# Kernel optimization log

Hardware: AMD Instinct MI355X
Metric: run time of the kernel (lower is better)

## Reference

```python
import jax, jax.numpy as jnp
import numpy as np

B, N, E = 2, 8192, 131072
IN_C, NF = 4, 32
F_IN = IN_C * NF          # 128, = in_channels * num_features
HID, H, OUT = 64, 8, 64   # hidden_features, nheads, out_features
NEG_SLOPE = 0.2           # GATv2Conv default negative_slope


def setup_inputs() -> dict:
    key = jax.random.key(0)
    ks = jax.random.split(key, 12)
    x = jax.random.normal(ks[0], (B, N, IN_C, NF), dtype=jnp.float32)
    edge_index = jax.random.randint(ks[1], (2, E), 0, N, dtype=jnp.int32)

    def w(k, shape, fan_in):
        return jax.random.normal(k, shape, dtype=jnp.float32) / np.sqrt(fan_in).astype(np.float32)

    # GATv2 layer 1: lin_l (source), lin_r (target), attention vector a, bias
    W1l = w(ks[2], (F_IN, H * HID), F_IN)
    W1r = w(ks[3], (F_IN, H * HID), F_IN)
    att1 = w(ks[4], (H, HID), HID)
    b1 = jnp.zeros((H * HID,), dtype=jnp.float32)
    # GATv2 layer 2: input channels = H*HID = 512
    W2l = w(ks[5], (H * HID, H * OUT), H * HID)
    W2r = w(ks[6], (H * HID, H * OUT), H * HID)
    att2 = w(ks[7], (H, OUT), OUT)
    b2 = jnp.zeros((H * OUT,), dtype=jnp.float32)
    return {"x": x, "edge_index": edge_index,
            "W1l": W1l, "W1r": W1r, "att1": att1, "b1": b1,
            "W2l": W2l, "W2r": W2r, "att2": att2, "b2": b2}


def _gatv2_layer(f, src, dst, Wl, Wr, att, b, heads, ch):
    # f: [N, F_in]; src/dst: [E'] (self-loops included)
    xl = (f @ Wl).reshape(N, heads, ch)   # source-side transform (messages)
    xr = (f @ Wr).reshape(N, heads, ch)   # target-side transform
    e = jax.nn.leaky_relu(xl[src] + xr[dst], NEG_SLOPE)     # [E', H, C]
    logits = jnp.einsum('ehc,hc->eh', e, att)               # [E', H]
    # softmax over incoming edges of each target node
    m = jax.lax.stop_gradient(jax.ops.segment_max(logits, dst, num_segments=N))
    a = jnp.exp(logits - m[dst])
    denom = jax.ops.segment_sum(a, dst, num_segments=N)     # [N, H] (>0: self-loops)
    a = a / denom[dst]
    out = jax.ops.segment_sum(xl[src] * a[:, :, None], dst, num_segments=N)
    return out.reshape(N, heads * ch) + b


def reference(x, edge_index, W1l, W1r, att1, b1, W2l, W2r, att2, b2):
    # add self-loops (PyG GATv2Conv default add_self_loops=True)
    loops = jnp.arange(N, dtype=edge_index.dtype)
    src = jnp.concatenate([edge_index[0], loops])
    dst = jnp.concatenate([edge_index[1], loops])
    feats = x.reshape(B, N, F_IN)  # view(batch, nodes, in_channels*num_features)

    def per_graph(f):
        h = _gatv2_layer(f, src, dst, W1l, W1r, att1, b1, H, HID)   # [N, 512]
        return _gatv2_layer(h, src, dst, W2l, W2r, att2, b2, H, OUT)  # [N, 512]

    h_prime = jax.vmap(per_graph)(feats)   # [B, N, H*OUT]
    return jax.nn.elu(h_prime)             # concat=True branch
```

## Files before the change

### kernel.cpp

```cpp
#include <hip/hip_runtime.h>
#include <cstdint>

#define NN 8192
#define NT 16384
#define EE 131072
#define EPAD (EE + NN)
#define SPAD (EPAD + 3 * NN)
#define FIN 128
#define CH 512
#define NH 8
#define NEG 0.2f

typedef __attribute__((ext_vector_type(8))) short short8;
typedef __attribute__((ext_vector_type(4))) unsigned short u16x4;
typedef __attribute__((ext_vector_type(4))) float f32x4;
typedef __attribute__((ext_vector_type(4))) int i32x4;

__device__ inline unsigned short bf16rne(float x) {
    unsigned u = __float_as_uint(x);
    unsigned r = (u + 0x7FFFu + ((u >> 16) & 1u)) >> 16;
    return (unsigned short)r;
}
__device__ inline float bf16tof(unsigned short h) {
    return __uint_as_float((unsigned)h << 16);
}
__device__ inline void gload16(const void* g, void* l) {
    __builtin_amdgcn_global_load_lds((const __attribute__((address_space(1))) void*)g,
                                     (__attribute__((address_space(3))) void*)l, 16, 0, 0);
}
template <int CTRL>
__device__ inline float dpp_add(float x) {
    int v = __builtin_amdgcn_update_dpp(0, __float_as_int(x), CTRL, 0xF, 0xF, true);
    return x + __int_as_float(v);
}


__global__ __launch_bounds__(256) void k_deg(const int* __restrict__ ei, int* __restrict__ deg) {
    int e = blockIdx.x * 256 + threadIdx.x;
    if (e >= EPAD) return;
    int dst = (e < EE) ? ei[EE + e] : (e - EE);
    atomicAdd(&deg[dst], 1);
}

__global__ __launch_bounds__(1024) void k_scan(const int* __restrict__ deg, int* __restrict__ rowptr) {
    __shared__ int part[1024];
    int t = threadIdx.x;
    int loc[8];
    int s = 0;
#pragma unroll
    for (int i = 0; i < 8; i++) { loc[i] = s; s += (deg[t * 8 + i] + 3) & ~3; }
    part[t] = s;
    __syncthreads();
    if (t == 0) {
        int run = 0;
        for (int i = 0; i < 1024; i++) { int tmp = part[i]; part[i] = run; run += tmp; }
        rowptr[NN] = run;
    }
    __syncthreads();
    int base = part[t];
#pragma unroll
    for (int i = 0; i < 8; i++) rowptr[t * 8 + i] = base + loc[i];
}

__global__ __launch_bounds__(256) void k_scatter(const int* __restrict__ ei, const int* __restrict__ rowptr,
                                                 int* __restrict__ cursor, int* __restrict__ ssrc) {
    int e = blockIdx.x * 256 + threadIdx.x;
    if (e >= EPAD) return;
    int src = (e < EE) ? ei[e] : (e - EE);
    int dst = (e < EE) ? ei[EE + e] : (e - EE);
    int pos = rowptr[dst] + atomicAdd(&cursor[dst], 1);
    ssrc[pos] = src;
}

__global__ __launch_bounds__(256) void k_pad(const int* __restrict__ rowptr, const int* __restrict__ deg,
                                             int* __restrict__ ssrc) {
    int n = blockIdx.x * 256 + threadIdx.x;
    if (n >= NN) return;
    int e = rowptr[n] + deg[n], pe = rowptr[n + 1];
    for (int i = e; i < pe; i++) ssrc[i] = 0;
}


__global__ __launch_bounds__(256) void k_cvt_ah(const float* __restrict__ F,
                                                unsigned short* __restrict__ Ah, int n4) {
    int i = blockIdx.x * 256 + threadIdx.x;
    if (i >= n4) return;
    f32x4 v = ((const f32x4*)F)[i];
#pragma unroll
    for (int c = 0; c < 4; c++) Ah[i * 4 + c] = bf16rne(v[c]);
}

template <int K>
__global__ __launch_bounds__(256) void k_cvt_w(const float* __restrict__ Wl, const float* __restrict__ Wr,
                                               unsigned short* __restrict__ Wh, unsigned short* __restrict__ Wlo) {
    int idx = blockIdx.x * 256 + threadIdx.x;
    int n = idx / K, k = idx % K;
    const float* W = (n < 512) ? Wl : Wr;
    float x = W[k * 512 + (n & 511)];
    unsigned short h = bf16rne(x);
    Wh[idx] = h;
    Wlo[idx] = bf16rne(x - bf16tof(h));
}


template <int K, int USE_BL, int BK>
__global__ __launch_bounds__(256) void k_gemm_mfma(const unsigned short* __restrict__ Ah,
                                                   const unsigned short* __restrict__ Bh,
                                                   const unsigned short* __restrict__ Bl,
                                                   unsigned short* __restrict__ XLb,
                                                   float* __restrict__ XR) {
    const int NS = BK / 8;
    __shared__ unsigned short sAh[NS][128][8], sBh[NS][128][8];
    __shared__ unsigned short sBl[USE_BL ? NS : 1][128][8];
    int tid = threadIdx.x;
    int l = tid & 63;
    int w = tid >> 6, wm = w >> 1, wn = w & 1;
    int m0 = blockIdx.x * 128, n0 = blockIdx.y * 128;
    int lr = l & 15, kh = l >> 4;
    f32x4 acc[4][4] = {};

    for (int k0 = 0; k0 < K; k0 += BK) {
#pragma unroll
        for (int g = 0; g < NS / 2; g++) {
            int cell = g * 256 + tid;
            int ckh = cell >> 7, cr = cell & 127;
            int ka = k0 + ckh * 8;
            gload16(Ah + (size_t)(m0 + cr) * K + ka, &sAh[ckh][cr][0]);
            gload16(Bh + (size_t)(n0 + cr) * K + ka, &sBh[ckh][cr][0]);
            if (USE_BL) gload16(Bl + (size_t)(n0 + cr) * K + ka, &sBl[ckh][cr][0]);
        }
        __syncthreads();
#pragma unroll
        for (int kk = 0; kk < BK / 32; kk++) {
            int ks = kk * 4 + kh;
            short8 fah[4], fbh[4], fbl[4];
#pragma unroll
            for (int i = 0; i < 4; i++) {
                fah[i] = *(const short8*)&sAh[ks][wm * 64 + i * 16 + lr][0];
                fbh[i] = *(const short8*)&sBh[ks][wn * 64 + i * 16 + lr][0];
                if (USE_BL) fbl[i] = *(const short8*)&sBl[ks][wn * 64 + i * 16 + lr][0];
            }
#pragma unroll
            for (int i = 0; i < 4; i++)
#pragma unroll
                for (int j = 0; j < 4; j++) {
                    if (USE_BL)
                        acc[i][j] = __builtin_amdgcn_mfma_f32_16x16x32_bf16(fah[i], fbl[j], acc[i][j], 0, 0, 0);
                    acc[i][j] = __builtin_amdgcn_mfma_f32_16x16x32_bf16(fah[i], fbh[j], acc[i][j], 0, 0, 0);
                }
        }
        __syncthreads();
    }
    int colt = n0 + wn * 64;
    int cb = colt & 511;
    if (colt < 512) {
#pragma unroll
        for (int i = 0; i < 4; i++) {
            int mg = m0 + wm * 64 + i * 16 + kh * 4;
#pragma unroll
            for (int j = 0; j < 4; j++) {
                int cg = cb + j * 16 + lr;
#pragma unroll
                for (int q = 0; q < 4; q++)
                    XLb[(size_t)(mg + q) * CH + cg] = bf16rne(acc[i][j][q]);
            }
        }
    } else {
#pragma unroll
        for (int i = 0; i < 4; i++) {
            int mg = m0 + wm * 64 + i * 16 + kh * 4;
#pragma unroll
            for (int j = 0; j < 4; j++) {
                int cg = cb + j * 16 + lr;
#pragma unroll
                for (int q = 0; q < 4; q++)
                    XR[(size_t)(mg + q) * CH + cg] = acc[i][j][q];
            }
        }
    }
}


#define GATHER(CX, IV)                                                         \
  {                                                                            \
    CX[0] = *(const u16x4*)(XLg + (size_t)IV[0] * CH);                         \
    CX[1] = *(const u16x4*)(XLg + (size_t)IV[1] * CH);                         \
    CX[2] = *(const u16x4*)(XLg + (size_t)IV[2] * CH);                         \
    CX[3] = *(const u16x4*)(XLg + (size_t)IV[3] * CH);                         \
  }

#define PROCESS(CX, cb)                                                        \
  {                                                                            \
    float f[4][4];                                                             \
    _Pragma("unroll") for (int e = 0; e < 4; e++)                              \
      _Pragma("unroll") for (int r = 0; r < 4; r++)                            \
        f[e][r] = bf16tof(CX[e][r]);                                           \
    float z[4];                                                                \
    _Pragma("unroll") for (int e = 0; e < 4; e++) {                            \
      float s = 0.f;                                                           \
      _Pragma("unroll") for (int r = 0; r < 4; r++) {                          \
        float t = f[e][r] + xrv[r];                                            \
        t = fmaxf(t, NEG * t);                                                 \
        s += t * atv[r];                                                       \
      }                                                                        \
      z[e] = s;                                                                \
    }                                                                          \
    _Pragma("unroll") for (int e = 0; e < 4; e++) {                            \
      z[e] = dpp_add<0xB1>(z[e]);                                              \
      z[e] = dpp_add<0x4E>(z[e]);                                              \
      z[e] = dpp_add<0x124>(z[e]);                                             \
      z[e] = dpp_add<0x128>(z[e]);                                             \
    }                                                                          \
    _Pragma("unroll") for (int e = 1; e < 4; e++)                              \
      if ((cb) + e >= end) z[e] = -1e30f;                                      \
    float mc = fmaxf(fmaxf(z[0], z[1]), fmaxf(z[2], z[3]));                    \
    if (__ballot(mc > mh + 8.f) == 0ULL) {                                     \
      float p0 = __expf(z[0] - mh), p1 = __expf(z[1] - mh);                    \
      float p2 = __expf(z[2] - mh), p3 = __expf(z[3] - mh);                    \
      sh += (p0 + p1) + (p2 + p3);                                             \
      _Pragma("unroll") for (int r = 0; r < 4; r++)                            \
        acc[r] += p0 * f[0][r] + p1 * f[1][r] + p2 * f[2][r] + p3 * f[3][r];   \
    } else {                                                                   \
      float nm = fmaxf(mh, mc);                                                \
      float sc = __expf(mh - nm);                                              \
      float p0 = __expf(z[0] - nm), p1 = __expf(z[1] - nm);                    \
      float p2 = __expf(z[2] - nm), p3 = __expf(z[3] - nm);                    \
      sh = sh * sc + (p0 + p1) + (p2 + p3);                                    \
      mh = nm;                                                                 \
      _Pragma("unroll") for (int r = 0; r < 4; r++)                            \
        acc[r] = acc[r] * sc + p0 * f[0][r] + p1 * f[1][r] + p2 * f[2][r] +    \
                 p3 * f[3][r];                                                 \
    }                                                                          \
  }

template <int WRITE_BF16>
__global__ __launch_bounds__(256) void k_node5(const unsigned short* __restrict__ XLb,
                                               const float* __restrict__ XR,
                                               const int* __restrict__ rowptr,
                                               const int* __restrict__ deg,
                                               const int* __restrict__ ssrc,
                                               const float* __restrict__ att,
                                               const float* __restrict__ bias,
                                               float* __restrict__ OUT,
                                               unsigned short* __restrict__ OAh) {
    int w = threadIdx.x >> 6;
    int nid = blockIdx.x * 2 + (w >> 1);
    int g = w & 1;
    int l = threadIdx.x & 63;
    int node = nid & (NN - 1);
    int beg = rowptr[node], pend = rowptr[node + 1];
    int end = beg + deg[node];
    int hb = g * 256 + l * 4;

    const unsigned short* XLg = XLb + (size_t)(nid >> 13) * NN * CH + hb;
    f32x4 xrv = *(const f32x4*)(XR + (size_t)nid * CH + hb);
    f32x4 atv = *(const f32x4*)(att + hb);
    f32x4 acc = {0.f, 0.f, 0.f, 0.f};
    float mh = -1e30f, sh = 0.f;

    i32x4 iA = *(const i32x4*)(ssrc + beg);
    i32x4 iB = iA;
    u16x4 curA[4], curB[4];
    GATHER(curA, iA);
    if (beg + 4 < pend) iB = *(const i32x4*)(ssrc + beg + 4);

    int base = beg;
    while (true) {
        if (base + 4 < pend) GATHER(curB, iB);
        if (base + 8 < pend) iA = *(const i32x4*)(ssrc + base + 8);
        PROCESS(curA, base);
        base += 4;
        if (base >= pend) break;
        if (base + 4 < pend) GATHER(curA, iA);
        if (base + 8 < pend) iB = *(const i32x4*)(ssrc + base + 8);
        PROCESS(curB, base);
        base += 4;
        if (base >= pend) break;
    }

    float inv = 1.f / sh;
    f32x4 biasv = *(const f32x4*)(bias + hb);
    size_t ob = (size_t)nid * CH + hb;
    if (WRITE_BF16) {
        u16x4 hv;
#pragma unroll
        for (int r = 0; r < 4; r++) {
            float wv = acc[r] * inv + biasv[r];
            hv[r] = bf16rne(wv);
        }
        *(u16x4*)(OAh + ob) = hv;
    } else {
        f32x4 ov;
#pragma unroll
        for (int r = 0; r < 4; r++) {
            float wv = acc[r] * inv + biasv[r];
            ov[r] = (wv > 0.f) ? wv : (__expf(wv) - 1.f);
        }
        *(f32x4*)(OUT + ob) = ov;
    }
}


extern "C" void kernel_launch(void* const* d_in, const int* in_sizes, int n_in,
                              void* d_out, int out_size, void* d_ws, size_t ws_size,
                              hipStream_t stream) {
    const float* x    = (const float*)d_in[0];
    const int*   ei   = (const int*)d_in[1];
    const float* W1l  = (const float*)d_in[2];
    const float* W1r  = (const float*)d_in[3];
    const float* att1 = (const float*)d_in[4];
    const float* b1   = (const float*)d_in[5];
    const float* W2l  = (const float*)d_in[6];
    const float* W2r  = (const float*)d_in[7];
    const float* att2 = (const float*)d_in[8];
    const float* b2   = (const float*)d_in[9];
    float* out = (float*)d_out;

    char* ws = (char*)d_ws;
    int* rowptr = (int*)ws;
    int* cursor = rowptr + NN + 1;
    int* deg    = cursor + NN;
    int* ssrc   = deg + NN;
    unsigned short* XLb = (unsigned short*)(((uintptr_t)(ssrc + SPAD) + 255) & ~(uintptr_t)255);
    float* XR = (float*)(XLb + (size_t)NT * CH);
    unsigned short* A_h = (unsigned short*)(XR + (size_t)NT * CH);
    unsigned short* W1h = A_h + (size_t)NT * CH;
    unsigned short* W1o = W1h + 1024 * FIN;
    unsigned short* W2h = W1o + 1024 * FIN;
    unsigned short* W2o = W2h + 1024 * CH;

    hipMemsetAsync(cursor, 0, (size_t)2 * NN * sizeof(int), stream);
    k_deg<<<(EPAD + 255) / 256, 256, 0, stream>>>(ei, deg);
    k_scan<<<1, 1024, 0, stream>>>(deg, rowptr);
    k_scatter<<<(EPAD + 255) / 256, 256, 0, stream>>>(ei, rowptr, cursor, ssrc);
    k_pad<<<NN / 256, 256, 0, stream>>>(rowptr, deg, ssrc);
    k_cvt_w<FIN><<<1024 * FIN / 256, 256, 0, stream>>>(W1l, W1r, W1h, W1o);
    k_cvt_w<CH><<<1024 * CH / 256, 256, 0, stream>>>(W2l, W2r, W2h, W2o);

    k_cvt_ah<<<NT * FIN / 4 / 256, 256, 0, stream>>>(x, A_h, NT * FIN / 4);
    k_gemm_mfma<FIN, 1, 32><<<dim3(NT / 128, 8), 256, 0, stream>>>(A_h, W1h, W1o, XLb, XR);
    k_node5<1><<<NT / 2, 256, 0, stream>>>(XLb, XR, rowptr, deg, ssrc, att1, b1, nullptr, A_h);
    k_gemm_mfma<CH, 0, 64><<<dim3(NT / 128, 8), 256, 0, stream>>>(A_h, W2h, W2o, XLb, XR);
    k_node5<0><<<NT / 2, 256, 0, stream>>>(XLb, XR, rowptr, deg, ssrc, att2, b2, out, nullptr);
}
```

Baseline: 221.9 us.

## Drop split-bf16 weight correction in layer-1 GEMM and warp-parallelize scan

Removes the hi/lo bf16 split for the layer-1 weights, so the first GEMM issues half the MFMAs and loads one B tile instead of two, and its K-tile grows to 64. The single-thread serial prefix sum in the row-pointer scan becomes a wavefront shuffle scan followed by a small cross-wave scan. The cost is lower precision in the layer-1 projection, since the weights are now plain bf16 and the correction term is gone.

Measured after the change: 210.9 us. 5.0% less time.

```diff
diff --git a/kernel.cpp b/kernel.cpp
--- a/kernel.cpp
+++ b/kernel.cpp
@@ -43,23 +43,36 @@
 }
 
 __global__ __launch_bounds__(1024) void k_scan(const int* __restrict__ deg, int* __restrict__ rowptr) {
-    __shared__ int part[1024];
+    __shared__ int wsum[16];
     int t = threadIdx.x;
+    int lane = t & 63, wid = t >> 6;
     int loc[8];
     int s = 0;
 #pragma unroll
     for (int i = 0; i < 8; i++) { loc[i] = s; s += (deg[t * 8 + i] + 3) & ~3; }
-    part[t] = s;
+    int inc = s;
+#pragma unroll
+    for (int off = 1; off < 64; off <<= 1) {
+        int v = __shfl_up(inc, off);
+        if (lane >= off) inc += v;
+    }
+    if (lane == 63) wsum[wid] = inc;
     __syncthreads();
-    if (t == 0) {
-        int run = 0;
-        for (int i = 0; i < 1024; i++) { int tmp = part[i]; part[i] = run; run += tmp; }
-        rowptr[NN] = run;
+    if (wid == 0 && lane < 16) {
+        int v = wsum[lane];
+#pragma unroll
+        for (int off = 1; off < 16; off <<= 1) {
+            int u = __shfl_up(v, off);
+            if (lane >= off) v += u;
+        }
+        wsum[lane] = v;
     }
     __syncthreads();
-    int base = part[t];
+    int wbase = (wid == 0) ? 0 : wsum[wid - 1];
+    int base = wbase + inc - s;
 #pragma unroll
     for (int i = 0; i < 8; i++) rowptr[t * 8 + i] = base + loc[i];
+    if (t == 1023) rowptr[NN] = wbase + inc;
 }
 
 __global__ __launch_bounds__(256) void k_scatter(const int* __restrict__ ei, const int* __restrict__ rowptr,
@@ -92,26 +105,21 @@
 
 template <int K>
 __global__ __launch_bounds__(256) void k_cvt_w(const float* __restrict__ Wl, const float* __restrict__ Wr,
-                                               unsigned short* __restrict__ Wh, unsigned short* __restrict__ Wlo) {
+                                               unsigned short* __restrict__ Wh) {
     int idx = blockIdx.x * 256 + threadIdx.x;
     int n = idx / K, k = idx % K;
     const float* W = (n < 512) ? Wl : Wr;
-    float x = W[k * 512 + (n & 511)];
-    unsigned short h = bf16rne(x);
-    Wh[idx] = h;
-    Wlo[idx] = bf16rne(x - bf16tof(h));
-}
-
-
-template <int K, int USE_BL, int BK>
+    Wh[idx] = bf16rne(W[k * 512 + (n & 511)]);
+}
+
+
+template <int K, int BK>
 __global__ __launch_bounds__(256) void k_gemm_mfma(const unsigned short* __restrict__ Ah,
                                                    const unsigned short* __restrict__ Bh,
-                                                   const unsigned short* __restrict__ Bl,
                                                    unsigned short* __restrict__ XLb,
                                                    float* __restrict__ XR) {
     const int NS = BK / 8;
     __shared__ unsigned short sAh[NS][128][8], sBh[NS][128][8];
-    __shared__ unsigned short sBl[USE_BL ? NS : 1][128][8];
     int tid = threadIdx.x;
     int l = tid & 63;
     int w = tid >> 6, wm = w >> 1, wn = w & 1;
@@ -127,27 +135,22 @@
             int ka = k0 + ckh * 8;
             gload16(Ah + (size_t)(m0 + cr) * K + ka, &sAh[ckh][cr][0]);
             gload16(Bh + (size_t)(n0 + cr) * K + ka, &sBh[ckh][cr][0]);
-            if (USE_BL) gload16(Bl + (size_t)(n0 + cr) * K + ka, &sBl[ckh][cr][0]);
         }
         __syncthreads();
 #pragma unroll
         for (int kk = 0; kk < BK / 32; kk++) {
             int ks = kk * 4 + kh;
-            short8 fah[4], fbh[4], fbl[4];
+            short8 fah[4], fbh[4];
 #pragma unroll
             for (int i = 0; i < 4; i++) {
                 fah[i] = *(const short8*)&sAh[ks][wm * 64 + i * 16 + lr][0];
                 fbh[i] = *(const short8*)&sBh[ks][wn * 64 + i * 16 + lr][0];
-                if (USE_BL) fbl[i] = *(const short8*)&sBl[ks][wn * 64 + i * 16 + lr][0];
             }
 #pragma unroll
             for (int i = 0; i < 4; i++)
 #pragma unroll
-                for (int j = 0; j < 4; j++) {
-                    if (USE_BL)
-                        acc[i][j] = __builtin_amdgcn_mfma_f32_16x16x32_bf16(fah[i], fbl[j], acc[i][j], 0, 0, 0);
+                for (int j = 0; j < 4; j++)
                     acc[i][j] = __builtin_amdgcn_mfma_f32_16x16x32_bf16(fah[i], fbh[j], acc[i][j], 0, 0, 0);
-                }
         }
         __syncthreads();
     }
@@ -325,21 +328,21 @@
     float* XR = (float*)(XLb + (size_t)NT * CH);
     unsigned short* A_h = (unsigned short*)(XR + (size_t)NT * CH);
     unsigned short* W1h = A_h + (size_t)NT * CH;
-    unsigned short* W1o = W1h + 1024 * FIN;
-    unsigned short* W2h = W1o + 1024 * FIN;
+    unsigned short* W2h = W1h + 1024 * FIN;
     unsigned short* W2o = W2h + 1024 * CH;
 
+    (void)W2o;
     hipMemsetAsync(cursor, 0, (size_t)2 * NN * sizeof(int), stream);
     k_deg<<<(EPAD + 255) / 256, 256, 0, stream>>>(ei, deg);
     k_scan<<<1, 1024, 0, stream>>>(deg, rowptr);
     k_scatter<<<(EPAD + 255) / 256, 256, 0, stream>>>(ei, rowptr, cursor, ssrc);
     k_pad<<<NN / 256, 256, 0, stream>>>(rowptr, deg, ssrc);
-    k_cvt_w<FIN><<<1024 * FIN / 256, 256, 0, stream>>>(W1l, W1r, W1h, W1o);
-    k_cvt_w<CH><<<1024 * CH / 256, 256, 0, stream>>>(W2l, W2r, W2h, W2o);
+    k_cvt_w<FIN><<<1024 * FIN / 256, 256, 0, stream>>>(W1l, W1r, W1h);
+    k_cvt_w<CH><<<1024 * CH / 256, 256, 0, stream>>>(W2l, W2r, W2h);
 
     k_cvt_ah<<<NT * FIN / 4 / 256, 256, 0, stream>>>(x, A_h, NT * FIN / 4);
-    k_gemm_mfma<FIN, 1, 32><<<dim3(NT / 128, 8), 256, 0, stream>>>(A_h, W1h, W1o, XLb, XR);
+    k_gemm_mfma<FIN, 64><<<dim3(NT / 128, 8), 256, 0, stream>>>(A_h, W1h, XLb, XR);
     k_node5<1><<<NT / 2, 256, 0, stream>>>(XLb, XR, rowptr, deg, ssrc, att1, b1, nullptr, A_h);
-    k_gemm_mfma<CH, 0, 64><<<dim3(NT / 128, 8), 256, 0, stream>>>(A_h, W2h, W2o, XLb, XR);
+    k_gemm_mfma<CH, 64><<<dim3(NT / 128, 8), 256, 0, stream>>>(A_h, W2h, XLb, XR);
     k_node5<0><<<NT / 2, 256, 0, stream>>>(XLb, XR, rowptr, deg, ssrc, att2, b2, out, nullptr);
 }
```
